# Kernel optimization log

Measured on AMD Instinct MI355X. Metric: run time of the kernel, lower is better.

Reference implementation:

```python
import jax, jax.numpy as jnp
import numpy as np

B, S, E, H = 8, 2048, 512, 8
HD = E // H
N_IND = 64


def setup_inputs() -> dict:
    key = jax.random.key(0)
    ks = jax.random.split(key, 10)
    s = 1.0 / np.sqrt(E)
    return {
        "x": jax.random.normal(ks[0], (B, S, E), jnp.float32),
        "Wq": jax.random.normal(ks[1], (E, E), jnp.float32) * s,
        "bq": jax.random.normal(ks[2], (E,), jnp.float32) * s,
        "Wk": jax.random.normal(ks[3], (E, E), jnp.float32) * s,
        "bk": jax.random.normal(ks[4], (E,), jnp.float32) * s,
        "Wv": jax.random.normal(ks[5], (E, E), jnp.float32) * s,
        "bv": jax.random.normal(ks[6], (E,), jnp.float32) * s,
        "Wo": jax.random.normal(ks[7], (E, E), jnp.float32) * s,
        "bo": jax.random.normal(ks[8], (E,), jnp.float32) * s,
        "industry_ids": jax.random.randint(ks[9], (S,), 0, N_IND, jnp.int32),
    }


def reference(x, Wq, bq, Wk, bk, Wv, bv, Wo, bo, industry_ids):
    # same-industry block mask [S, S]; every row attends at least to itself
    mask = industry_ids[:, None] == industry_ids[None, :]
    # projections (torch Linear: y = x @ W.T + b)
    q = (x @ Wq.T + bq).reshape(B, S, H, HD).transpose(0, 2, 1, 3)  # [B,H,S,HD]
    k = (x @ Wk.T + bk).reshape(B, S, H, HD).transpose(0, 2, 1, 3)
    v = (x @ Wv.T + bv).reshape(B, S, H, HD).transpose(0, 2, 1, 3)
    scores = jnp.einsum("bhqd,bhkd->bhqk", q, k) / np.sqrt(HD).astype(jnp.float32)
    scores = jnp.where(mask[None, None, :, :], scores, -jnp.inf)
    attn = jax.nn.softmax(scores, axis=-1)  # dropout is identity at inference
    out = jnp.einsum("bhqk,bhkd->bhqd", attn, v)
    out = out.transpose(0, 2, 1, 3).reshape(B, S, E)
    return out @ Wo.T + bo
```

## Files before the change

kernel.cpp:

```cpp
#include <hip/hip_runtime.h>
#include <cstdint>

#define DEVFN __device__ __forceinline__

typedef __bf16 bf16x8 __attribute__((ext_vector_type(8)));
typedef float f32x4 __attribute__((ext_vector_type(4)));
typedef unsigned int uint;

constexpr int Bc = 8, Sc = 2048, Ec = 512, Hc = 8, HDc = 64, NI = 64;
constexpr int Mtot = Bc * Sc;
constexpr int Kdim = Ec;
constexpr int MAXITEMS = 128;

DEVFN unsigned short f2bf(float f) {
  unsigned u = __builtin_bit_cast(unsigned, f);
  u += 0x7fffu + ((u >> 16) & 1u);
  return (unsigned short)(u >> 16);
}

typedef const void __attribute__((address_space(1))) gvoid_t;
typedef void __attribute__((address_space(3))) lvoid_t;
DEVFN void gload16(const void* g, void* l) {
  __builtin_amdgcn_global_load_lds((gvoid_t*)g, (lvoid_t*)l, 16, 0, 0);
}

DEVFN uint cvtpk(float lo, float hi) {
  uint r;
  asm("v_cvt_pk_bf16_f32 %0, %1, %2" : "=v"(r) : "v"(lo), "v"(hi));
  return r;
}

#define WAIT_VM_BARRIER(N)                                            \
  do {                                                                \
    asm volatile("s_waitcnt vmcnt(" #N ")\n\ts_barrier" ::: "memory"); \
    __builtin_amdgcn_sched_barrier(0);                                \
  } while (0)
#define WAIT_LGKM_BARRIER()                                            \
  do {                                                                 \
    asm volatile("s_waitcnt lgkmcnt(0)\n\ts_barrier" ::: "memory");    \
    __builtin_amdgcn_sched_barrier(0);                                 \
  } while (0)

__global__ void prep_kernel(const int* __restrict__ ids, int* __restrict__ perm,
                            int* __restrict__ gstart, int* __restrict__ gsz,
                            int* __restrict__ items, int* __restrict__ nitems,
                            const float* __restrict__ Wq, const float* __restrict__ Wk,
                            const float* __restrict__ Wv, const float* __restrict__ Wo,
                            ushort* __restrict__ Wcat, ushort* __restrict__ Wob) {
  if (blockIdx.x == 0) {
    __shared__ int sid[Sc];
    __shared__ int hist[NI];
    __shared__ int base[NI];
    int t = threadIdx.x;
    if (t < NI) hist[t] = 0;
    for (int i = t; i < Sc; i += 256) sid[i] = ids[i];
    __syncthreads();
    for (int i = t; i < Sc; i += 256) atomicAdd(&hist[sid[i]], 1);
    __syncthreads();
    if (t == 0) {
      int run = 0;
      for (int g = 0; g < NI; ++g) { base[g] = run; run += hist[g]; }
      int cnt = 0;
      for (int g = 0; g < NI; ++g)
        for (int q0 = 0; q0 < hist[g]; q0 += 32) items[cnt++] = (g << 16) | q0;
      *nitems = cnt;
    }
    __syncthreads();
    if (t < NI) { gstart[t] = base[t]; gsz[t] = hist[t]; }
    int lane = t & 63, w = t >> 6;
    for (int g = w; g < NI; g += 4) {
      int run = base[g];
      for (int c = 0; c < Sc; c += 64) {
        int tok = c + lane;
        int id = sid[tok];
        unsigned long long mask = __ballot(id == g);
        if (id == g) {
          int rank = __popcll(mask & ((1ull << lane) - 1ull));
          perm[run + rank] = tok;
        }
        run += __popcll(mask);
      }
    }
  } else {
    int i = (blockIdx.x - 1) * 256 + threadIdx.x;
    int idx = i * 4;
    int n = idx >> 9, k = idx & 511;
    const float* src;
    ushort* dst;
    if (n < 512)       { src = Wq + (size_t)n * 512 + k;          dst = Wcat + (size_t)n * 512 + k; }
    else if (n < 1024) { src = Wk + (size_t)(n - 512) * 512 + k;  dst = Wcat + (size_t)n * 512 + k; }
    else if (n < 1536) { src = Wv + (size_t)(n - 1024) * 512 + k; dst = Wcat + (size_t)n * 512 + k; }
    else               { src = Wo + (size_t)(n - 1536) * 512 + k; dst = Wob + (size_t)(n - 1536) * 512 + k; }
    float4 v = *(const float4*)src;
    ushort4 o = {f2bf(v.x), f2bf(v.y), f2bf(v.z), f2bf(v.w)};
    *(ushort4*)dst = o;
  }
}

__global__ void cvt_x_kernel(const float* __restrict__ x, const int* __restrict__ perm,
                             ushort* __restrict__ xb) {
  int i = blockIdx.x * 256 + threadIdx.x;
  int mp = i >> 7;
  int c = i & 127;
  int b = mp >> 11, p = mp & (Sc - 1);
  int srow = (b << 11) | perm[p];
  float4 v = *(const float4*)(x + (size_t)srow * Ec + c * 4);
  ushort4 o = {f2bf(v.x), f2bf(v.y), f2bf(v.z), f2bf(v.w)};
  ((ushort4*)xb)[i] = o;
}

__global__ __launch_bounds__(256) void gemm_qkv128(
    const ushort* __restrict__ A, const ushort* __restrict__ Bw,
    const float* __restrict__ bias0, const float* __restrict__ bias1,
    const float* __restrict__ bias2, ushort* __restrict__ qkvout) {
  constexpr int NK = Kdim / 64;
  __shared__ __align__(16) char ldsraw[65536];
  ushort* sAb = (ushort*)ldsraw;
  ushort* sBb = (ushort*)(ldsraw + 32768);
  const int tid = threadIdx.x;
  const int lane = tid & 63;
  const int wave = tid >> 6;
  const int wr = wave >> 1, wc = wave & 1;
  const int orig = blockIdx.x;
  const int xcd = orig & 7, gl = orig >> 3;
  const int mbase = (xcd * 16 + (gl & 15)) * 128;
  const int nbase = (gl >> 4) * 128;

  f32x4 acc[4][4] = {};

  const int rowS = wave * 32 + (lane >> 3);
  const int kc = lane & 7;

  auto stage = [&](int buf, int kt) {
    const int k0 = kt * 64;
#pragma unroll
    for (int c = 0; c < 4; ++c) {
      int row = rowS + c * 8;
      int kcp = (kc ^ (row & 7)) * 8;
      gload16(A + (size_t)(mbase + row) * Kdim + k0 + kcp,
              sAb + buf * 8192 + (wave * 256 + c * 64) * 8);
      gload16(Bw + (size_t)(nbase + row) * Kdim + k0 + kcp,
              sBb + buf * 8192 + (wave * 256 + c * 64) * 8);
    }
  };

  stage(0, 0);
  stage(1, 1);

  for (int kt = 0; kt < NK; ++kt) {
    const int cur = kt & 1;
    if (kt < NK - 1) {
      WAIT_VM_BARRIER(8);
    } else {
      WAIT_VM_BARRIER(0);
    }

    const char* Ab = (const char*)(sAb + cur * 8192);
    const char* Bb = (const char*)(sBb + cur * 8192);
    __builtin_amdgcn_s_setprio(1);
#pragma unroll
    for (int kk = 0; kk < 2; ++kk) {
      bf16x8 af[4], bfv[4];
#pragma unroll
      for (int i = 0; i < 4; ++i) {
        int row = wr * 64 + i * 16 + (lane & 15);
        int off = row * 128 + kk * 64 + (lane >> 4) * 16;
        off ^= (row & 7) << 4;
        af[i] = *(const bf16x8*)(Ab + off);
      }
#pragma unroll
      for (int j = 0; j < 4; ++j) {
        int col = wc * 64 + j * 16 + (lane & 15);
        int off = col * 128 + kk * 64 + (lane >> 4) * 16;
        off ^= (col & 7) << 4;
        bfv[j] = *(const bf16x8*)(Bb + off);
      }
#pragma unroll
      for (int i = 0; i < 4; ++i)
#pragma unroll
        for (int j = 0; j < 4; ++j)
          acc[i][j] = __builtin_amdgcn_mfma_f32_16x16x32_bf16(af[i], bfv[j], acc[i][j], 0, 0, 0);
    }
    __builtin_amdgcn_s_setprio(0);

    WAIT_LGKM_BARRIER();
    if (kt + 2 < NK) stage(cur, kt + 2);
  }

  {
    ushort* T = (ushort*)ldsraw;
#pragma unroll
    for (int i = 0; i < 4; ++i) {
#pragma unroll
      for (int j = 0; j < 4; ++j) {
        int nl = wc * 64 + j * 16 + (lane & 15);
        int n = nbase + nl;
        float bv = (n < 512) ? bias0[n] : (n < 1024) ? bias1[n - 512] : bias2[n - 1024];
#pragma unroll
        for (int r = 0; r < 4; ++r) {
          int ml = wr * 64 + i * 16 + (lane >> 4) * 4 + r;
          T[ml * 136 + nl] = f2bf(acc[i][j][r] + bv);
        }
      }
    }
    __syncthreads();
#pragma unroll
    for (int k = 0; k < 8; ++k) {
      int c = tid + 256 * k;
      int row = c >> 4, col8 = (c & 15) * 8;
      uint4 w = *(const uint4*)(T + row * 136 + col8);
      int n0 = nbase + col8;
      int proj = n0 >> 9, h = (n0 >> 6) & 7, d0 = n0 & 63;
      int p = mbase + row;
      int bidx = p >> 11, pl = p & (Sc - 1);
      size_t off = (size_t)proj * ((size_t)Bc * Hc * Sc * HDc) +
                   (size_t)((bidx * Hc + h) * Sc + pl) * HDc + d0;
      *(uint4*)(qkvout + off) = w;
    }
  }
}

__global__ __launch_bounds__(256) void gemm_out128(
    const ushort* __restrict__ A, const ushort* __restrict__ Bw,
    const float* __restrict__ bias0, const int* __restrict__ permarg,
    float* __restrict__ out) {
  constexpr int NK = Kdim / 64;
  constexpr int NTOT = 512;
  __shared__ __align__(16) char ldsraw[65536];
  ushort* sAb = (ushort*)ldsraw;
  ushort* sBb = (ushort*)(ldsraw + 32768);
  const int tid = threadIdx.x;
  const int lane = tid & 63;
  const int wave = tid >> 6;
  const int wr = wave >> 1, wc = wave & 1;
  const int orig = blockIdx.x;
  const int xcd = orig & 7, gl = orig >> 3;
  const int mbase = (xcd * 16 + (gl & 15)) * 128;
  const int nbase = (gl >> 4) * 128;

  f32x4 acc[4][4] = {};

  const int rowS = wave * 32 + (lane >> 3);
  const int kc = lane & 7;

  auto stage = [&](int buf, int kt) {
    const int k0 = kt * 64;
#pragma unroll
    for (int c = 0; c < 4; ++c) {
      int row = rowS + c * 8;
      int kcp = (kc ^ (row & 7)) * 8;
      gload16(A + (size_t)(mbase + row) * Kdim + k0 + kcp,
              sAb + buf * 8192 + (wave * 256 + c * 64) * 8);
      gload16(Bw + (size_t)(nbase + row) * Kdim + k0 + kcp,
              sBb + buf * 8192 + (wave * 256 + c * 64) * 8);
    }
  };

  stage(0, 0);
  stage(1, 1);

  for (int kt = 0; kt < NK; ++kt) {
    const int cur = kt & 1;
    if (kt < NK - 1) {
      WAIT_VM_BARRIER(8);
    } else {
      WAIT_VM_BARRIER(0);
    }

    const char* Ab = (const char*)(sAb + cur * 8192);
    const char* Bb = (const char*)(sBb + cur * 8192);
    __builtin_amdgcn_s_setprio(1);
#pragma unroll
    for (int kk = 0; kk < 2; ++kk) {
      bf16x8 af[4], bfv[4];
#pragma unroll
      for (int i = 0; i < 4; ++i) {
        int row = wr * 64 + i * 16 + (lane & 15);
        int off = row * 128 + kk * 64 + (lane >> 4) * 16;
        off ^= (row & 7) << 4;
        af[i] = *(const bf16x8*)(Ab + off);
      }
#pragma unroll
      for (int j = 0; j < 4; ++j) {
        int col = wc * 64 + j * 16 + (lane & 15);
        int off = col * 128 + kk * 64 + (lane >> 4) * 16;
        off ^= (col & 7) << 4;
        bfv[j] = *(const bf16x8*)(Bb + off);
      }
#pragma unroll
      for (int i = 0; i < 4; ++i)
#pragma unroll
        for (int j = 0; j < 4; ++j)
          acc[i][j] = __builtin_amdgcn_mfma_f32_16x16x32_bf16(af[i], bfv[j], acc[i][j], 0, 0, 0);
    }
    __builtin_amdgcn_s_setprio(0);

    WAIT_LGKM_BARRIER();
    if (kt + 2 < NK) stage(cur, kt + 2);
  }

  float* T = (float*)ldsraw;
#pragma unroll
  for (int i = 0; i < 4; ++i) {
#pragma unroll
    for (int j = 0; j < 4; ++j) {
      int nl = wc * 64 + j * 16 + (lane & 15);
      float bv = bias0[nbase + nl];
#pragma unroll
      for (int r = 0; r < 4; ++r) {
        int ml = wr * 64 + i * 16 + (lane >> 4) * 4 + r;
        T[ml * 128 + nl] = acc[i][j][r] + bv;
      }
    }
  }
  __syncthreads();
#pragma unroll
  for (int k = 0; k < 16; ++k) {
    int c = tid + 256 * k;
    int row = c >> 5, col4 = (c & 31) * 4;
    float4 w = *(const float4*)(T + row * 128 + col4);
    int p = mbase + row;
    int bidx = p >> 11;
    int orow = (bidx << 11) | permarg[p & (Sc - 1)];
    *(float4*)(out + (size_t)orow * NTOT + nbase + col4) = w;
  }
}

__global__ __launch_bounds__(64) void attn5_kernel(
    const ushort* __restrict__ qkv, const int* __restrict__ gstart,
    const int* __restrict__ gsz, const int* __restrict__ items,
    const int* __restrict__ nitems, ushort* __restrict__ obuf) {
  __shared__ __align__(16) ushort vt[64 * 40];
  if ((int)blockIdx.x >= *nitems) return;
  const int iv = items[blockIdx.x];
  const int g = iv >> 16, q0 = iv & 0xffff;
  const int bh = blockIdx.y;
  const int start = gstart[g], n = gsz[g];
  const int lane = threadIdx.x;
  const int ql = lane & 15, lg = lane >> 4;

  const size_t planeSz = (size_t)Bc * Hc * Sc * HDc;
  const ushort* qb = qkv + (size_t)bh * Sc * HDc;
  const ushort* kb = qb + planeSz;
  const ushort* vb = kb + planeSz;

  bf16x8 qf[2][2];
#pragma unroll
  for (int qt = 0; qt < 2; ++qt) {
    int row = min(start + q0 + qt * 16 + ql, Sc - 1);
#pragma unroll
    for (int h = 0; h < 2; ++h)
      qf[qt][h] = *(const bf16x8*)(qb + (size_t)row * HDc + h * 32 + lg * 8);
  }

  f32x4 oacc[2][4] = {};
  float lsum[2] = {0.f, 0.f};

  const int vk = lane & 31;
  const int vh = (lane >> 5) * 32;
  const int Lbase = 4 * (ql + 32 * (lg & 1));

  const int npair = (n + 31) >> 5;
  for (int pr = 0; pr < npair; ++pr) {
    const int c0 = pr * 32;
    int vrow = min(start + c0 + vk, Sc - 1);
    const uint4* vp = (const uint4*)(vb + (size_t)vrow * HDc + vh);
    uint4 v0 = vp[0], v1 = vp[1], v2 = vp[2], v3 = vp[3];

    bf16x8 kf[2][2];
#pragma unroll
    for (int t = 0; t < 2; ++t) {
      int row = min(start + c0 + t * 16 + ql, Sc - 1);
#pragma unroll
      for (int h = 0; h < 2; ++h)
        kf[t][h] = *(const bf16x8*)(kb + (size_t)row * HDc + h * 32 + lg * 8);
    }

    uint pw[2][4];
#pragma unroll
    for (int qt = 0; qt < 2; ++qt) {
      f32x4 s0 = {}, s1 = {};
      s0 = __builtin_amdgcn_mfma_f32_16x16x32_bf16(kf[0][0], qf[qt][0], s0, 0, 0, 0);
      s0 = __builtin_amdgcn_mfma_f32_16x16x32_bf16(kf[0][1], qf[qt][1], s0, 0, 0, 0);
      s1 = __builtin_amdgcn_mfma_f32_16x16x32_bf16(kf[1][0], qf[qt][0], s1, 0, 0, 0);
      s1 = __builtin_amdgcn_mfma_f32_16x16x32_bf16(kf[1][1], qf[qt][1], s1, 0, 0, 0);
      float p0[4], p1[4];
      float ls = 0.f;
#pragma unroll
      for (int r = 0; r < 4; ++r) {
        int kk = c0 + 4 * lg + r;
        float e0 = (kk < n) ? __expf(s0[r] * 0.125f) : 0.f;
        float e1 = (kk + 16 < n) ? __expf(s1[r] * 0.125f) : 0.f;
        p0[r] = e0;
        p1[r] = e1;
        ls += e0 + e1;
      }
      lsum[qt] += ls;
      uint a0 = cvtpk(p0[0], p0[1]), b0 = cvtpk(p0[2], p0[3]);
      uint a1 = cvtpk(p1[0], p1[1]), b1 = cvtpk(p1[2], p1[3]);
      uint pA0 = __builtin_amdgcn_ds_bpermute(Lbase, a0);
      uint pB0 = __builtin_amdgcn_ds_bpermute(Lbase, b0);
      uint pA1 = __builtin_amdgcn_ds_bpermute(Lbase, a1);
      uint pB1 = __builtin_amdgcn_ds_bpermute(Lbase, b1);
      uint pC0 = __builtin_amdgcn_ds_bpermute(Lbase + 64, a0);
      uint pD0 = __builtin_amdgcn_ds_bpermute(Lbase + 64, b0);
      uint pC1 = __builtin_amdgcn_ds_bpermute(Lbase + 64, a1);
      uint pD1 = __builtin_amdgcn_ds_bpermute(Lbase + 64, b1);
      bool t0 = lg < 2;
      pw[qt][0] = t0 ? pA0 : pA1;
      pw[qt][1] = t0 ? pB0 : pB1;
      pw[qt][2] = t0 ? pC0 : pC1;
      pw[qt][3] = t0 ? pD0 : pD1;
    }

    {
      uint w[16] = {v0.x, v0.y, v0.z, v0.w, v1.x, v1.y, v1.z, v1.w,
                    v2.x, v2.y, v2.z, v2.w, v3.x, v3.y, v3.z, v3.w};
#pragma unroll
      for (int i = 0; i < 16; ++i) {
        vt[(vh + 2 * i) * 40 + vk] = (ushort)(w[i] & 0xffffu);
        vt[(vh + 2 * i + 1) * 40 + vk] = (ushort)(w[i] >> 16);
      }
    }
    asm volatile("s_waitcnt lgkmcnt(0)" ::: "memory");
    __builtin_amdgcn_sched_barrier(0);
    bf16x8 vf[4];
#pragma unroll
    for (int dq = 0; dq < 4; ++dq)
      vf[dq] = *(const bf16x8*)(vt + (dq * 16 + ql) * 40 + lg * 8);
    asm volatile("s_waitcnt lgkmcnt(0)" ::: "memory");
    __builtin_amdgcn_sched_barrier(0);
#pragma unroll
    for (int qt = 0; qt < 2; ++qt) {
      union { uint u[4]; bf16x8 v; } pf;
      pf.u[0] = pw[qt][0]; pf.u[1] = pw[qt][1]; pf.u[2] = pw[qt][2]; pf.u[3] = pw[qt][3];
#pragma unroll
      for (int dq = 0; dq < 4; ++dq)
        oacc[qt][dq] = __builtin_amdgcn_mfma_f32_16x16x32_bf16(vf[dq], pf.v, oacc[qt][dq], 0, 0, 0);
    }
  }

#pragma unroll
  for (int qt = 0; qt < 2; ++qt) {
    float l = lsum[qt];
    l += __shfl_xor(l, 16);
    l += __shfl_xor(l, 32);
    float inv = 1.f / l;
    int qi = q0 + qt * 16 + ql;
    if (qi < n) {
      int p = start + qi;
      ushort* op = obuf + (size_t)((bh >> 3) * Sc + p) * Ec + (bh & 7) * HDc + lg * 4;
#pragma unroll
      for (int dq = 0; dq < 4; ++dq) {
        uint w0 = cvtpk(oacc[qt][dq][0] * inv, oacc[qt][dq][1] * inv);
        uint w1 = cvtpk(oacc[qt][dq][2] * inv, oacc[qt][dq][3] * inv);
        uint2 wv = {w0, w1};
        *(uint2*)(op + dq * 16) = wv;
      }
    }
  }
}

extern "C" void kernel_launch(void* const* d_in, const int* in_sizes, int n_in,
                              void* d_out, int out_size, void* d_ws, size_t ws_size,
                              hipStream_t stream) {
  const float* x  = (const float*)d_in[0];
  const float* Wq = (const float*)d_in[1];
  const float* bq = (const float*)d_in[2];
  const float* Wk = (const float*)d_in[3];
  const float* bk = (const float*)d_in[4];
  const float* Wv = (const float*)d_in[5];
  const float* bv = (const float*)d_in[6];
  const float* Wo = (const float*)d_in[7];
  const float* bo = (const float*)d_in[8];
  const int* ids  = (const int*)d_in[9];
  float* out = (float*)d_out;

  char* ws = (char*)d_ws;
  ushort* xb   = (ushort*)(ws);
  ushort* Wcat = (ushort*)(ws + 16777216);
  ushort* Wob  = (ushort*)(ws + 18350080);
  ushort* qkv  = (ushort*)(ws + 18874368);
  ushort* obuf = (ushort*)(ws + 69206016);
  int* perm    = (int*)(ws + 85983232);
  int* gstart  = perm + Sc;
  int* gsz     = gstart + NI;
  int* items   = gsz + NI;
  int* nitems  = items + MAXITEMS;

  prep_kernel<<<dim3(1 + 2048 * 512 / 4 / 256), dim3(256), 0, stream>>>(
      ids, perm, gstart, gsz, items, nitems, Wq, Wk, Wv, Wo, Wcat, Wob);
  cvt_x_kernel<<<dim3(Mtot * Ec / 4 / 256), dim3(256), 0, stream>>>(x, perm, xb);
  gemm_qkv128<<<dim3(Mtot / 128 * 12), dim3(256), 0, stream>>>(xb, Wcat, bq, bk, bv, qkv);
  attn5_kernel<<<dim3(MAXITEMS, Bc * Hc), dim3(64), 0, stream>>>(qkv, gstart, gsz, items,
                                                                 nitems, obuf);
  gemm_out128<<<dim3(Mtot / 128 * 4), dim3(256), 0, stream>>>(obuf, Wob, bo, perm, out);
}
```

Baseline: 127.5 us.

## Fold x bf16 conversion into prep kernel and gather permuted rows in QKV GEMM

The x-to-bf16 conversion moves into the prep kernel as extra blocks that convert x in its original order, so the separate cvt_x launch and its dependency on perm go away. The QKV GEMM now applies the industry permutation itself, looking up perm once per staged row and loading A rows through that index. This removes one kernel launch and lets the x conversion overlap with the permutation build. The cost is that A-tile loads in the GEMM become scattered row gathers, which may hurt locality.

```diff
diff --git a/kernel.cpp b/kernel.cpp
--- a/kernel.cpp
+++ b/kernel.cpp
@@ -41,12 +41,13 @@
     __builtin_amdgcn_sched_barrier(0);                                 \
   } while (0)
 
-__global__ void prep_kernel(const int* __restrict__ ids, int* __restrict__ perm,
-                            int* __restrict__ gstart, int* __restrict__ gsz,
-                            int* __restrict__ items, int* __restrict__ nitems,
-                            const float* __restrict__ Wq, const float* __restrict__ Wk,
-                            const float* __restrict__ Wv, const float* __restrict__ Wo,
-                            ushort* __restrict__ Wcat, ushort* __restrict__ Wob) {
+__global__ void prep2_kernel(const int* __restrict__ ids, int* __restrict__ perm,
+                             int* __restrict__ gstart, int* __restrict__ gsz,
+                             int* __restrict__ items, int* __restrict__ nitems,
+                             const float* __restrict__ Wq, const float* __restrict__ Wk,
+                             const float* __restrict__ Wv, const float* __restrict__ Wo,
+                             ushort* __restrict__ Wcat, ushort* __restrict__ Wob,
+                             const float* __restrict__ x, ushort* __restrict__ xb) {
   if (blockIdx.x == 0) {
     __shared__ int sid[Sc];
     __shared__ int hist[NI];
@@ -81,7 +82,7 @@
         run += __popcll(mask);
       }
     }
-  } else {
+  } else if (blockIdx.x <= 1024) {
     int i = (blockIdx.x - 1) * 256 + threadIdx.x;
     int idx = i * 4;
     int n = idx >> 9, k = idx & 511;
@@ -94,25 +95,19 @@
     float4 v = *(const float4*)src;
     ushort4 o = {f2bf(v.x), f2bf(v.y), f2bf(v.z), f2bf(v.w)};
     *(ushort4*)dst = o;
-  }
-}
-
-__global__ void cvt_x_kernel(const float* __restrict__ x, const int* __restrict__ perm,
-                             ushort* __restrict__ xb) {
-  int i = blockIdx.x * 256 + threadIdx.x;
-  int mp = i >> 7;
-  int c = i & 127;
-  int b = mp >> 11, p = mp & (Sc - 1);
-  int srow = (b << 11) | perm[p];
-  float4 v = *(const float4*)(x + (size_t)srow * Ec + c * 4);
-  ushort4 o = {f2bf(v.x), f2bf(v.y), f2bf(v.z), f2bf(v.w)};
-  ((ushort4*)xb)[i] = o;
+  } else {
+    int i = (blockIdx.x - 1025) * 256 + threadIdx.x;
+    float4 v = ((const float4*)x)[i];
+    ushort4 o = {f2bf(v.x), f2bf(v.y), f2bf(v.z), f2bf(v.w)};
+    ((ushort4*)xb)[i] = o;
+  }
 }
 
 __global__ __launch_bounds__(256) void gemm_qkv128(
     const ushort* __restrict__ A, const ushort* __restrict__ Bw,
     const float* __restrict__ bias0, const float* __restrict__ bias1,
-    const float* __restrict__ bias2, ushort* __restrict__ qkvout) {
+    const float* __restrict__ bias2, const int* __restrict__ permarg,
+    ushort* __restrict__ qkvout) {
   constexpr int NK = Kdim / 64;
   __shared__ __align__(16) char ldsraw[65536];
   ushort* sAb = (ushort*)ldsraw;
@@ -130,6 +125,12 @@
 
   const int rowS = wave * 32 + (lane >> 3);
   const int kc = lane & 7;
+  const int mb_hi = mbase & ~(Sc - 1);
+
+  int arow[4];
+#pragma unroll
+  for (int c = 0; c < 4; ++c)
+    arow[c] = mb_hi | permarg[(mbase + rowS + c * 8) & (Sc - 1)];
 
   auto stage = [&](int buf, int kt) {
     const int k0 = kt * 64;
@@ -137,7 +138,7 @@
     for (int c = 0; c < 4; ++c) {
       int row = rowS + c * 8;
       int kcp = (kc ^ (row & 7)) * 8;
-      gload16(A + (size_t)(mbase + row) * Kdim + k0 + kcp,
+      gload16(A + (size_t)arow[c] * Kdim + k0 + kcp,
               sAb + buf * 8192 + (wave * 256 + c * 64) * 8);
       gload16(Bw + (size_t)(nbase + row) * Kdim + k0 + kcp,
               sBb + buf * 8192 + (wave * 256 + c * 64) * 8);
@@ -488,10 +489,9 @@
   int* items   = gsz + NI;
   int* nitems  = items + MAXITEMS;
 
-  prep_kernel<<<dim3(1 + 2048 * 512 / 4 / 256), dim3(256), 0, stream>>>(
-      ids, perm, gstart, gsz, items, nitems, Wq, Wk, Wv, Wo, Wcat, Wob);
-  cvt_x_kernel<<<dim3(Mtot * Ec / 4 / 256), dim3(256), 0, stream>>>(x, perm, xb);
-  gemm_qkv128<<<dim3(Mtot / 128 * 12), dim3(256), 0, stream>>>(xb, Wcat, bq, bk, bv, qkv);
+  prep2_kernel<<<dim3(1 + 1024 + Mtot * Ec / 4 / 256), dim3(256), 0, stream>>>(
+      ids, perm, gstart, gsz, items, nitems, Wq, Wk, Wv, Wo, Wcat, Wob, x, xb);
+  gemm_qkv128<<<dim3(Mtot / 128 * 12), dim3(256), 0, stream>>>(xb, Wcat, bq, bk, bv, perm, qkv);
   attn5_kernel<<<dim3(MAXITEMS, Bc * Hc), dim3(64), 0, stream>>>(qkv, gstart, gsz, items,
                                                                  nitems, obuf);
   gemm_out128<<<dim3(Mtot / 128 * 4), dim3(256), 0, stream>>>(obuf, Wob, bo, perm, out);
```

New measurement: 118.4 us, median of 2. 1.08x faster.
